# Performance work log

Measured on AMD Instinct MI355X. Metric: run time of the kernel, lower is better.

## Reference

```python
import jax, jax.numpy as jnp
import numpy as np

NHEADS = 64; EMB = 2048; STATE = 128; KCONV = 4; NGROUPS = 1
HEAD_DIM = 64; CHUNK = 128; EPS = 1e-6
INTER = NHEADS * HEAD_DIM                  # int(expand*emb_dim) = 4096
CONV_DIM = INTER + 2 * NGROUPS * STATE     # 4352
PROJ = INTER + CONV_DIM + NHEADS           # 8512
BATCH = 2; SEQ = 2048


def segsum(x):
    # x: (..., T) -> (..., T, T) stable segment sums; -inf strictly above diagonal
    T = x.shape[-1]
    xe = jnp.broadcast_to(x[..., None], x.shape + (T,))
    m_strict = jnp.tril(jnp.ones((T, T), bool), -1)
    s = jnp.cumsum(jnp.where(m_strict, xe, 0.0), axis=-2)
    m_incl = jnp.tril(jnp.ones((T, T), bool), 0)
    return jnp.where(m_incl, s, -jnp.inf)


def setup_inputs() -> dict:
    key = jax.random.key(0)
    ks = jax.random.split(key, 6)
    x = jax.random.normal(ks[0], (BATCH, SEQ, EMB), jnp.float32)
    in_proj_w = jax.random.normal(ks[1], (PROJ, EMB), jnp.float32) * 0.02
    conv_w = jax.random.normal(ks[2], (CONV_DIM, 1, KCONV), jnp.float32) * 0.2
    conv_b = jax.random.normal(ks[3], (CONV_DIM,), jnp.float32) * 0.1
    dt_bias = jnp.ones((NHEADS,), jnp.float32)
    A_log = jnp.log(jnp.arange(1, NHEADS + 1, dtype=jnp.float32))
    D = jnp.ones((NHEADS,), jnp.float32)
    norm_w = jnp.ones((INTER,), jnp.float32)
    out_proj_w = jax.random.normal(ks[4], (EMB, INTER), jnp.float32) * 0.02
    mask = jnp.ones((BATCH, 1, SEQ), jnp.int32)  # shape[1]==1 -> masking is a no-op, as in torch path
    return {"x": x, "in_proj_w": in_proj_w, "conv_w": conv_w, "conv_b": conv_b,
            "dt_bias": dt_bias, "A_log": A_log, "D": D, "norm_w": norm_w,
            "out_proj_w": out_proj_w, "mask": mask}


def reference(x, in_proj_w, conv_w, conv_b, dt_bias, A_log, D, norm_w, out_proj_w, mask):
    b, s, _ = x.shape
    proj = x @ in_proj_w.T                                    # (b,s,PROJ)
    gate = proj[..., :INTER]
    hBC = proj[..., INTER:INTER + CONV_DIM]
    dt = proj[..., INTER + CONV_DIM:]                         # (b,s,H)

    # causal depthwise conv1d (torch pads k-1 both sides then truncates to seq_len == left-pad k-1)
    conv = jax.lax.conv_general_dilated(
        hBC.transpose(0, 2, 1), conv_w, (1,), [(KCONV - 1, 0)],
        feature_group_count=CONV_DIM)
    hBC = jax.nn.silu((conv + conv_b[None, :, None]).transpose(0, 2, 1))

    hid = hBC[..., :INTER]
    Bm = hBC[..., INTER:INTER + NGROUPS * STATE]
    Cm = hBC[..., INTER + NGROUPS * STATE:]

    A = -jnp.exp(A_log)                                       # (H,)
    dt = jax.nn.softplus(dt + dt_bias)                        # clamp(0,inf) is a no-op after softplus

    hid = hid.reshape(b, s, NHEADS, HEAD_DIM)
    pad = (CHUNK - s % CHUNK) % CHUNK
    D_res = D[:, None] * jnp.pad(hid, ((0, 0), (0, pad), (0, 0), (0, 0)))
    hid = hid * dt[..., None]
    A_s = A * dt                                              # (b,s,H)
    Bm = jnp.tile(Bm.reshape(b, s, NGROUPS, STATE), (1, 1, NHEADS // NGROUPS, 1))
    Cm = jnp.tile(Cm.reshape(b, s, NGROUPS, STATE), (1, 1, NHEADS // NGROUPS, 1))

    def chunkify(t):
        t = jnp.pad(t, ((0, 0), (0, pad)) + ((0, 0),) * (t.ndim - 2))
        return t.reshape(b, -1, CHUNK, *t.shape[2:])

    hid_c, A_c, B_c, C_c = (chunkify(t) for t in (hid, A_s, Bm, Cm))
    A_c = A_c.transpose(0, 3, 1, 2)                           # (b,H,c,l)
    A_cum = jnp.cumsum(A_c, -1)

    # intra-chunk (diagonal blocks)
    L = jnp.exp(segsum(A_c))                                  # (b,H,c,l,l)
    G = jnp.einsum('bclhn,bcshn->bhcls', C_c, B_c)
    Y_diag = jnp.einsum('bhcls,bcshp->bclhp', G * L, hid_c)

    # per-chunk end states
    decay_states = jnp.exp(A_cum[..., -1:] - A_cum)           # (b,H,c,l)
    states = jnp.einsum('bclhn,bhcl,bclhp->bchpn', B_c, decay_states, hid_c)

    # inter-chunk recurrence
    A_last = jnp.pad(A_cum[..., -1], ((0, 0), (0, 0), (1, 0)))  # (b,H,c+1)
    decay_chunk = jnp.exp(segsum(A_last))                     # (b,H,c+1,c+1)
    states = jnp.concatenate([jnp.zeros_like(states[:, :1]), states], axis=1)
    new_states = jnp.einsum('bhzc,bchpn->bzhpn', decay_chunk, states)
    states = new_states[:, :-1]                               # states entering each chunk

    # off-diagonal (cross-chunk) contribution
    state_decay = jnp.exp(A_cum)                              # (b,H,c,l)
    Y_off = jnp.einsum('bclhn,bchpn,bhcl->bclhp', C_c, states, state_decay)

    y = (Y_diag + Y_off).reshape(b, -1, NHEADS, HEAD_DIM) + D_res
    y = y[:, :s].reshape(b, s, INTER)

    # gated RMSNorm
    yg = y * jax.nn.silu(gate)
    yn = norm_w * (yg * jax.lax.rsqrt(jnp.mean(yg * yg, -1, keepdims=True) + EPS))
    return yn @ out_proj_w.T
```

## Files before the change

kernel.cpp:

```cpp
#include <hip/hip_runtime.h>
#include <math.h>

#define NHEADS   64
#define EMB      2048
#define STATE    128
#define KCONV    4
#define HEAD_DIM 64
#define CHUNK    128
#define SEQL     2048
#define NBATCH   2
#define NCH      (SEQL/CHUNK)
#define INTER    (NHEADS*HEAD_DIM)
#define CONVD    (INTER + 2*STATE)
#define PROJD    (INTER + CONVD + NHEADS)
#define ROWS     (NBATCH*SEQL)
#define EPSV     1e-6f

__device__ __forceinline__ float sigmoidf_(float x){ return 1.f/(1.f+__expf(-x)); }

__device__ __forceinline__ float b2f(ushort u){
  union{float f; unsigned u;} x; x.u = ((unsigned)u)<<16; return x.f;
}
__device__ __forceinline__ ushort f2b(float f){
  union{float f; unsigned u;} x; x.f=f;
  unsigned r = x.u + 0x7FFFu + ((x.u>>16)&1u);
  return (ushort)(r>>16);
}
__device__ __forceinline__ float4 ld4(const float* p){ return *(const float4*)p; }
__device__ __forceinline__ float4 ld4(const ushort* p){
  ushort4 v = *(const ushort4*)p;
  return make_float4(b2f(v.x),b2f(v.y),b2f(v.z),b2f(v.w));
}
__device__ __forceinline__ void st4(float* p, float4 v){ *(float4*)p = v; }
__device__ __forceinline__ void st4(ushort* p, float4 v){
  ushort4 o; o.x=f2b(v.x); o.y=f2b(v.y); o.z=f2b(v.z); o.w=f2b(v.w);
  *(ushort4*)p = o;
}
__device__ __forceinline__ void stc(float* p, float v){ *p = v; }
__device__ __forceinline__ void stc(ushort* p, float v){ *p = f2b(v); }

__global__ __launch_bounds__(256) void f32_to_bf16_kernel(
    const float* __restrict__ in, ushort* __restrict__ out, long n)
{
  long i = ((long)blockIdx.x*256 + threadIdx.x) * 8;
  if (i >= n) return;
  float4 a = *(const float4*)(in + i);
  float4 b = *(const float4*)(in + i + 4);
  st4(out + i, a);
  st4(out + i + 4, b);
}

typedef __attribute__((ext_vector_type(8))) short short8v;
typedef __attribute__((ext_vector_type(4))) float float4v;

#define GLL16(g, l) __builtin_amdgcn_global_load_lds( \
    (const __attribute__((address_space(1))) void*)(g), \
    (__attribute__((address_space(3))) void*)(l), 16, 0, 0)

template<typename TC>
__global__ __launch_bounds__(256) void gemm_mfma_bt(
    const ushort* __restrict__ A, int lda,
    const ushort* __restrict__ B, int ldb,
    TC* __restrict__ C, int ldc,
    int N, int K)
{
  __shared__ ushort As[2][128*32];
  __shared__ ushort Bs[2][128*32];
  const int t = threadIdx.x;
  const int lt = t & 63, w = t >> 6;
  const int wr = w >> 1, wc = w & 1;

  const int nwg = gridDim.x * gridDim.y;
  int orig = blockIdx.x + gridDim.x * blockIdx.y;
  int tile = orig;
  if ((nwg & 7) == 0) tile = (orig & 7) * (nwg >> 3) + (orig >> 3);
  const int m0 = (tile / gridDim.x) * 128;
  const int n0 = (tile % gridDim.x) * 128;

  float4v acc[4][4];
  #pragma unroll
  for (int i=0;i<4;++i)
    #pragma unroll
    for (int j=0;j<4;++j) acc[i][j] = float4v{0.f,0.f,0.f,0.f};

  const int srow = t >> 2;
  const int scol = ((t & 3) ^ ((srow >> 1) & 3)) * 8;
  const int bn0 = min(n0 + srow, N-1);
  const int bn1 = min(n0 + 64 + srow, N-1);
  const long aoff0 = (long)(m0 + srow) * lda + scol;
  const long aoff1 = (long)(m0 + 64 + srow) * lda + scol;
  const long boff0 = (long)bn0 * ldb + scol;
  const long boff1 = (long)bn1 * ldb + scol;
  const int lr = lt & 15, lks = lt >> 4;

  for (int k0 = 0; k0 < K; k0 += 64) {
    GLL16(A + aoff0 + k0,      As[0] + t*8);
    GLL16(A + aoff1 + k0,      As[0] + 2048 + t*8);
    GLL16(B + boff0 + k0,      Bs[0] + t*8);
    GLL16(B + boff1 + k0,      Bs[0] + 2048 + t*8);
    GLL16(A + aoff0 + k0 + 32, As[1] + t*8);
    GLL16(A + aoff1 + k0 + 32, As[1] + 2048 + t*8);
    GLL16(B + boff0 + k0 + 32, Bs[1] + t*8);
    GLL16(B + boff1 + k0 + 32, Bs[1] + 2048 + t*8);
    __syncthreads();
    #pragma unroll
    for (int hB = 0; hB < 2; ++hB) {
      short8v af[4], bf[4];
      #pragma unroll
      for (int i = 0; i < 4; ++i) {
        int ra = wr*64 + i*16 + lr;
        af[i] = *(const short8v*)(As[hB] + ra*32 + ((lks ^ ((ra>>1)&3)) << 3));
        int rb = wc*64 + i*16 + lr;
        bf[i] = *(const short8v*)(Bs[hB] + rb*32 + ((lks ^ ((rb>>1)&3)) << 3));
      }
      #pragma unroll
      for (int i = 0; i < 4; ++i)
        #pragma unroll
        for (int j = 0; j < 4; ++j)
          acc[i][j] = __builtin_amdgcn_mfma_f32_16x16x32_bf16(af[i], bf[j], acc[i][j], 0, 0, 0);
    }
    __syncthreads();
  }

  const int cr = (lt >> 4) * 4;
  const int cc = lt & 15;
  #pragma unroll
  for (int i = 0; i < 4; ++i) {
    #pragma unroll
    for (int j = 0; j < 4; ++j) {
      int col = n0 + wc*64 + j*16 + cc;
      if (col < N) {
        #pragma unroll
        for (int r = 0; r < 4; ++r) {
          int row = m0 + wr*64 + i*16 + cr + r;
          stc(C + (long)row*ldc + col, acc[i][j][r]);
        }
      }
    }
  }
}

__global__ __launch_bounds__(256) void g_mfma_kernel(
    const ushort* __restrict__ conv, float* __restrict__ G)
{
  const int bc = blockIdx.x;
  const long r0 = (long)bc*CHUNK;
  __shared__ ushort Cs[128][136];
  __shared__ ushort Bs[128][136];
  const int t = threadIdx.x;
  const int lt = t & 63, w = t >> 6;
  const int lr = lt & 15, lk = (lt >> 4) * 8;

  for (int i = t; i < 128*16; i += 256) {
    int r = i >> 4, n0 = (i & 15) * 8;
    *(short8v*)&Cs[r][n0] = *(const short8v*)(conv + (r0+r)*CONVD + INTER + STATE + n0);
    *(short8v*)&Bs[r][n0] = *(const short8v*)(conv + (r0+r)*CONVD + INTER + n0);
  }
  __syncthreads();

  float4v acc[2][8];
  #pragma unroll
  for (int m=0;m<2;++m)
    #pragma unroll
    for (int j=0;j<8;++j) acc[m][j] = float4v{0,0,0,0};
  #pragma unroll
  for (int kk = 0; kk < 4; ++kk) {
    short8v a0 = *(const short8v*)&Cs[w*32 +      lr][kk*32 + lk];
    short8v a1 = *(const short8v*)&Cs[w*32 + 16 + lr][kk*32 + lk];
    #pragma unroll
    for (int nj = 0; nj < 8; ++nj) {
      short8v bv = *(const short8v*)&Bs[nj*16 + lr][kk*32 + lk];
      acc[0][nj] = __builtin_amdgcn_mfma_f32_16x16x32_bf16(a0, bv, acc[0][nj], 0, 0, 0);
      acc[1][nj] = __builtin_amdgcn_mfma_f32_16x16x32_bf16(a1, bv, acc[1][nj], 0, 0, 0);
    }
  }
  float* Gb = G + (long)bc*CHUNK*CHUNK;
  const int cr = (lt >> 4) * 4, cc = lt & 15;
  #pragma unroll
  for (int m = 0; m < 2; ++m)
    #pragma unroll
    for (int nj = 0; nj < 8; ++nj)
      #pragma unroll
      for (int r = 0; r < 4; ++r)
        Gb[(w*32 + m*16 + cr + r)*CHUNK + nj*16 + cc] = acc[m][nj][r];
}

__global__ __launch_bounds__(256) void conv_silu_kernel(
    const ushort* __restrict__ proj, const float* __restrict__ cw,
    const float* __restrict__ cb, ushort* __restrict__ out)
{
  const int C4 = CONVD/4;
  long idx = (long)blockIdx.x*256 + threadIdx.x;
  if (idx >= (long)ROWS*C4) return;
  int r = (int)(idx / C4);
  int c = (int)(idx % C4) * 4;
  int tt = r & (SEQL-1);
  float4 bv = *(const float4*)(cb + c);
  float acc0=bv.x, acc1=bv.y, acc2=bv.z, acc3=bv.w;
  float4 w0 = *(const float4*)(cw + (c+0)*KCONV);
  float4 w1 = *(const float4*)(cw + (c+1)*KCONV);
  float4 w2 = *(const float4*)(cw + (c+2)*KCONV);
  float4 w3 = *(const float4*)(cw + (c+3)*KCONV);
  const float wj0[4] = {w0.x,w0.y,w0.z,w0.w};
  const float wj1[4] = {w1.x,w1.y,w1.z,w1.w};
  const float wj2[4] = {w2.x,w2.y,w2.z,w2.w};
  const float wj3[4] = {w3.x,w3.y,w3.z,w3.w};
  #pragma unroll
  for (int j = 0; j < KCONV; ++j) {
    int tr = tt - (KCONV-1) + j;
    if (tr >= 0) {
      float4 v = ld4(proj + (long)(r - (KCONV-1) + j)*PROJD + INTER + c);
      acc0 = fmaf(v.x, wj0[j], acc0);
      acc1 = fmaf(v.y, wj1[j], acc1);
      acc2 = fmaf(v.z, wj2[j], acc2);
      acc3 = fmaf(v.w, wj3[j], acc3);
    }
  }
  float4 o;
  o.x = acc0 * sigmoidf_(acc0);
  o.y = acc1 * sigmoidf_(acc1);
  o.z = acc2 * sigmoidf_(acc2);
  o.w = acc3 * sigmoidf_(acc3);
  st4(out + (long)r*CONVD + c, o);
}

__global__ __launch_bounds__(256) void dt_acum_kernel(
    const ushort* __restrict__ proj, const float* __restrict__ dt_bias,
    const float* __restrict__ A_log, float* __restrict__ dtb,
    float* __restrict__ acum)
{
  const int bc = blockIdx.x;
  const long r0 = (long)bc*CHUNK;
  __shared__ float dts[CHUNK][NHEADS+1];
  const int t = threadIdx.x;
  for (int i = t; i < CHUNK*8; i += 256) {
    int l = i >> 3, h0 = (i & 7) * 8;
    short8v v = *(const short8v*)(proj + (r0+l)*PROJD + INTER + CONVD + h0);
    #pragma unroll
    for (int j = 0; j < 8; ++j) {
      float xv = b2f((ushort)v[j]) + dt_bias[h0+j];
      float sp = fmaxf(xv, 0.f) + __logf(1.f + __expf(-fabsf(xv)));
      dts[l][h0+j] = sp;
      dtb[(r0+l)*NHEADS + h0 + j] = sp;
    }
  }
  __syncthreads();
  if (t < NHEADS) {
    float Ah = -__expf(A_log[t]);
    float acc = 0.f;
    float* o = acum + ((long)bc*NHEADS + t)*CHUNK;
    for (int l = 0; l < CHUNK; ++l) { acc = fmaf(Ah, dts[l][t], acc); o[l] = acc; }
  }
}

__global__ __launch_bounds__(256) void states_mfma_kernel(
    const ushort* __restrict__ conv, const float* __restrict__ dtb,
    const float* __restrict__ acum, ushort* __restrict__ states)
{
  const int h = blockIdx.x, c = blockIdx.y, b = blockIdx.z;
  const int bc = b*NCH + c;
  const long r0 = (long)bc*CHUNK;
  __shared__ ushort Ahi[64][136];
  __shared__ ushort Alo[64][136];
  __shared__ ushort Bt[128][136];
  __shared__ float arow[CHUNK];
  __shared__ float wrow[CHUNK];
  const int t = threadIdx.x;
  const int lt = t & 63, w = t >> 6;
  const int lr = lt & 15, lk = (lt >> 4) * 8;

  if (t < CHUNK) arow[t] = acum[((long)bc*NHEADS + h)*CHUNK + t];
  __syncthreads();
  if (t < CHUNK) wrow[t] = dtb[(r0 + t)*NHEADS + h] * __expf(arow[CHUNK-1] - arow[t]);
  __syncthreads();

  for (int i = t; i < CHUNK*HEAD_DIM/8; i += 256) {
    int l = i >> 3, p0 = (i & 7) * 8;
    short8v v = *(const short8v*)(conv + (r0+l)*CONVD + h*HEAD_DIM + p0);
    float wl = wrow[l];
    #pragma unroll
    for (int j = 0; j < 8; ++j) {
      float f = b2f((ushort)v[j]) * wl;
      ushort hb = f2b(f);
      Ahi[p0+j][l] = hb;
      Alo[p0+j][l] = f2b(f - b2f(hb));
    }
  }
  for (int i = t; i < CHUNK*STATE/8; i += 256) {
    int l = i >> 4, n0 = (i & 15) * 8;
    short8v v = *(const short8v*)(conv + (r0+l)*CONVD + INTER + n0);
    #pragma unroll
    for (int j = 0; j < 8; ++j) Bt[n0+j][l] = (ushort)v[j];
  }
  __syncthreads();

  float4v acc[8];
  #pragma unroll
  for (int j = 0; j < 8; ++j) acc[j] = float4v{0,0,0,0};
  #pragma unroll
  for (int kk = 0; kk < 4; ++kk) {
    short8v ahi = *(const short8v*)&Ahi[w*16 + lr][kk*32 + lk];
    short8v alo = *(const short8v*)&Alo[w*16 + lr][kk*32 + lk];
    #pragma unroll
    for (int nj = 0; nj < 8; ++nj) {
      short8v bv = *(const short8v*)&Bt[nj*16 + lr][kk*32 + lk];
      acc[nj] = __builtin_amdgcn_mfma_f32_16x16x32_bf16(ahi, bv, acc[nj], 0, 0, 0);
      acc[nj] = __builtin_amdgcn_mfma_f32_16x16x32_bf16(alo, bv, acc[nj], 0, 0, 0);
    }
  }
  ushort* so = states + ((long)bc*NHEADS + h)*HEAD_DIM*STATE;
  const int cr = (lt >> 4) * 4, cc = lt & 15;
  #pragma unroll
  for (int nj = 0; nj < 8; ++nj)
    #pragma unroll
    for (int r = 0; r < 4; ++r)
      so[(w*16 + cr + r)*STATE + nj*16 + cc] = f2b(acc[nj][r]);
}

__global__ __launch_bounds__(256) void scan_kernel(
    ushort* __restrict__ states, const float* __restrict__ acum)
{
  const int blk = blockIdx.x;
  const int bh = blk >> 2, pq = blk & 3;
  const int b = bh >> 6, h = bh & 63;
  const int t = threadIdx.x;
  const int base = pq * 16 * STATE;
  float acc[8];
  #pragma unroll
  for (int i=0;i<8;++i) acc[i]=0.f;
  for (int c = 0; c < NCH; ++c) {
    const long bch = ((long)(b*NCH + c)*NHEADS + h);
    float lam = __expf(acum[bch*CHUNK + CHUNK-1]);
    ushort* sb = states + bch*HEAD_DIM*STATE + base;
    #pragma unroll
    for (int i = 0; i < 8; ++i) {
      float v = b2f(sb[t + i*256]);
      sb[t + i*256] = f2b(acc[i]);
      acc[i] = fmaf(acc[i], lam, v);
    }
  }
}

__global__ __launch_bounds__(256) void y_mfma_kernel(
    const ushort* __restrict__ conv, const float* __restrict__ dtb,
    const float* __restrict__ acum, const float* __restrict__ G,
    const ushort* __restrict__ states, const float* __restrict__ Dp,
    ushort* __restrict__ proj)
{
  const int h = blockIdx.x;
  const int c = blockIdx.y >> 1, mh = blockIdx.y & 1;
  const int b = blockIdx.z;
  const int bc = b*NCH + c;
  const int mbase = mh * 64;
  const long r0 = (long)bc*CHUNK;

  __shared__ float  Af[64][132];
  __shared__ ushort B0[64][136];
  __shared__ ushort B1[64][136];
  __shared__ float arow[CHUNK];
  __shared__ float dtr[CHUNK];
  __shared__ float el[64];

  const int t = threadIdx.x;
  const int lt = t & 63, w = t >> 6;
  const int lr = lt & 15, lk = (lt >> 4) * 8;

  if (t < CHUNK) {
    arow[t] = acum[((long)bc*NHEADS + h)*CHUNK + t];
    dtr[t]  = dtb[(r0 + t)*NHEADS + h];
  }
  __syncthreads();

  if (t < 64) el[t] = __expf(arow[mbase + t]);
  for (int i = t; i < CHUNK*HEAD_DIM/8; i += 256) {
    int s = i >> 3, p0 = (i & 7) * 8;
    short8v v = *(const short8v*)(conv + (r0+s)*CONVD + h*HEAD_DIM + p0);
    #pragma unroll
    for (int j = 0; j < 8; ++j) B0[p0+j][s] = (ushort)v[j];
  }
  {
    const ushort* stb = states + ((long)bc*NHEADS + h)*HEAD_DIM*STATE;
    for (int i = t; i < HEAD_DIM*STATE/8; i += 256) {
      int p = i >> 4, n0 = (i & 15) * 8;
      *(short8v*)&B1[p][n0] = *(const short8v*)(stb + p*STATE + n0);
    }
  }
  {
    const float* Gb = G + (long)bc*CHUNK*CHUNK;
    for (int i = t; i < 64*CHUNK; i += 256) {
      int ll = i >> 7, s = i & 127;
      int l = mbase + ll;
      float wv = 0.f;
      if (s <= l) wv = Gb[l*CHUNK + s] * __expf(arow[l] - arow[s]) * dtr[s];
      Af[ll][s] = wv;
    }
  }
  __syncthreads();

  float4v acc1[4], acc2[4];
  #pragma unroll
  for (int j = 0; j < 4; ++j) { acc1[j] = float4v{0,0,0,0}; acc2[j] = float4v{0,0,0,0}; }

  #pragma unroll
  for (int kk = 0; kk < 4; ++kk) {
    const float* ap = &Af[w*16 + lr][kk*32 + lk];
    float a8[8];
    *(float4*)&a8[0] = *(const float4*)ap;
    *(float4*)&a8[4] = *(const float4*)(ap + 4);
    short8v ahi, alo;
    #pragma unroll
    for (int e = 0; e < 8; ++e) {
      ushort hb = f2b(a8[e]);
      float rem = a8[e] - b2f(hb);
      ahi[e] = (short)hb;
      alo[e] = (short)f2b(rem);
    }
    #pragma unroll
    for (int nj = 0; nj < 4; ++nj) {
      short8v bfv = *(const short8v*)&B0[nj*16 + lr][kk*32 + lk];
      acc1[nj] = __builtin_amdgcn_mfma_f32_16x16x32_bf16(ahi, bfv, acc1[nj], 0, 0, 0);
      acc1[nj] = __builtin_amdgcn_mfma_f32_16x16x32_bf16(alo, bfv, acc1[nj], 0, 0, 0);
    }
  }
  __syncthreads();

  for (int i = t; i < 64*STATE; i += 256) {
    int ll = i >> 7, n = i & 127;
    Af[ll][n] = b2f(conv[(r0 + mbase + ll)*CONVD + INTER + STATE + n]);
  }
  __syncthreads();

  #pragma unroll
  for (int kk = 0; kk < 4; ++kk) {
    const float* ap = &Af[w*16 + lr][kk*32 + lk];
    float a8[8];
    *(float4*)&a8[0] = *(const float4*)ap;
    *(float4*)&a8[4] = *(const float4*)(ap + 4);
    short8v ahi;
    #pragma unroll
    for (int e = 0; e < 8; ++e) ahi[e] = (short)f2b(a8[e]);
    #pragma unroll
    for (int nj = 0; nj < 4; ++nj) {
      short8v bfv = *(const short8v*)&B1[nj*16 + lr][kk*32 + lk];
      acc2[nj] = __builtin_amdgcn_mfma_f32_16x16x32_bf16(ahi, bfv, acc2[nj], 0, 0, 0);
    }
  }

  const float Dh = Dp[h];
  const int cr = (lt >> 4) * 4, cc = lt & 15;
  #pragma unroll
  for (int nj = 0; nj < 4; ++nj) {
    int p = nj*16 + cc;
    #pragma unroll
    for (int r = 0; r < 4; ++r) {
      int ll = w*16 + cr + r;
      float hid_raw = b2f(B0[p][mbase + ll]);
      float yv = acc1[nj][r] + el[ll]*acc2[nj][r] + Dh*hid_raw;
      proj[(r0 + mbase + ll)*PROJD + INTER + h*HEAD_DIM + p] = f2b(yv);
    }
  }
}

__global__ __launch_bounds__(256) void gate_norm_kernel(
    ushort* __restrict__ proj, const float* __restrict__ nw)
{
  const int r = blockIdx.x;
  const int t = threadIdx.x;
  __shared__ float red[256];
  ushort* gate = proj + (long)r*PROJD;
  ushort* y = gate + INTER;
  float vals[16];
  float ss = 0.f;
  #pragma unroll
  for (int k = 0; k < 4; ++k) {
    int j = (t + k*256) * 4;
    float4 g = ld4(gate + j);
    float4 yv = ld4(y + j);
    float v0 = yv.x * g.x * sigmoidf_(g.x);
    float v1 = yv.y * g.y * sigmoidf_(g.y);
    float v2 = yv.z * g.z * sigmoidf_(g.z);
    float v3 = yv.w * g.w * sigmoidf_(g.w);
    vals[k*4+0]=v0; vals[k*4+1]=v1; vals[k*4+2]=v2; vals[k*4+3]=v3;
    ss += v0*v0 + v1*v1 + v2*v2 + v3*v3;
  }
  red[t] = ss;
  __syncthreads();
  for (int sft = 128; sft > 0; sft >>= 1) {
    if (t < sft) red[t] += red[t+sft];
    __syncthreads();
  }
  float scale = rsqrtf(red[0] / (float)INTER + EPSV);
  #pragma unroll
  for (int k = 0; k < 4; ++k) {
    int j = (t + k*256) * 4;
    float4 w = *(const float4*)(nw + j);
    st4(y + j, make_float4(vals[k*4+0]*scale*w.x, vals[k*4+1]*scale*w.y,
                           vals[k*4+2]*scale*w.z, vals[k*4+3]*scale*w.w));
  }
}

extern "C" void kernel_launch(void* const* d_in, const int* in_sizes, int n_in,
                              void* d_out, int out_size, void* d_ws, size_t ws_size,
                              hipStream_t stream) {
  const float* x       = (const float*)d_in[0];
  const float* Wi      = (const float*)d_in[1];
  const float* cw      = (const float*)d_in[2];
  const float* cb      = (const float*)d_in[3];
  const float* dt_bias = (const float*)d_in[4];
  const float* A_log   = (const float*)d_in[5];
  const float* Dp      = (const float*)d_in[6];
  const float* nw      = (const float*)d_in[7];
  const float* Wo      = (const float*)d_in[8];
  float* out = (float*)d_out;

  ushort* projb = (ushort*)d_ws;
  ushort* R     = projb + (size_t)ROWS*PROJD;
  ushort* xb    = R;
  ushort* Wib   = R + (size_t)ROWS*EMB;
  ushort* Wob   = R;
  ushort* convb = R;
  float*  dtb   = (float*)(convb + (size_t)ROWS*CONVD);
  float*  acum  = dtb  + (size_t)ROWS*NHEADS;
  float*  Gb    = acum + (size_t)NBATCH*NCH*NHEADS*CHUNK;
  ushort* st    = (ushort*)(Gb + (size_t)NBATCH*NCH*CHUNK*CHUNK);

  size_t need = (size_t)ROWS*PROJD*2 + (size_t)ROWS*CONVD*2
              + (size_t)ROWS*NHEADS*4 + (size_t)NBATCH*NCH*NHEADS*CHUNK*4
              + (size_t)NBATCH*NCH*CHUNK*CHUNK*4
              + (size_t)NBATCH*NCH*NHEADS*HEAD_DIM*STATE*2;
  if (ws_size < need) return;

  f32_to_bf16_kernel<<<(int)((long)ROWS*EMB/8/256), 256, 0, stream>>>(x, xb, (long)ROWS*EMB);
  f32_to_bf16_kernel<<<(int)((long)PROJD*EMB/8/256), 256, 0, stream>>>(Wi, Wib, (long)PROJD*EMB);
  gemm_mfma_bt<ushort><<<dim3((PROJD+127)/128, ROWS/128), 256, 0, stream>>>(
      xb, EMB, Wib, EMB, projb, PROJD, PROJD, EMB);
  conv_silu_kernel<<<(int)(((long)ROWS*(CONVD/4)+255)/256), 256, 0, stream>>>(
      projb, cw, cb, convb);
  dt_acum_kernel<<<NBATCH*NCH, 256, 0, stream>>>(projb, dt_bias, A_log, dtb, acum);
  g_mfma_kernel<<<NBATCH*NCH, 256, 0, stream>>>(convb, Gb);
  states_mfma_kernel<<<dim3(NHEADS, NCH, NBATCH), 256, 0, stream>>>(convb, dtb, acum, st);
  scan_kernel<<<NBATCH*NHEADS*4, 256, 0, stream>>>(st, acum);
  y_mfma_kernel<<<dim3(NHEADS, NCH*2, NBATCH), 256, 0, stream>>>(
      convb, dtb, acum, Gb, st, Dp, projb);
  gate_norm_kernel<<<ROWS, 256, 0, stream>>>(projb, nw);
  f32_to_bf16_kernel<<<(int)((long)EMB*INTER/8/256), 256, 0, stream>>>(Wo, Wob, (long)EMB*INTER);
  gemm_mfma_bt<float><<<dim3(EMB/128, ROWS/128), 256, 0, stream>>>(
      projb + INTER, PROJD, Wob, INTER, out, EMB, EMB, INTER);
}
```

Baseline: 590.2 us.

## Vectorize MFMA epilogue stores, merge conversions, fold y kernel halves

Swaps the MFMA operand order in every matmul so each lane holds four consecutive output columns, which lets the epilogues issue one vector store instead of four scalar ones. The two fp32-to-bf16 conversions for x and the input weights are merged into a single launch. The y kernel now processes a whole chunk per block, loading the per-head operands once for both 64-row halves, and skips the causally zero K-steps in the first half. The cost is fewer blocks and more serialized work per block in the y kernel.

```diff
diff --git a/kernel.cpp b/kernel.cpp
--- a/kernel.cpp
+++ b/kernel.cpp
@@ -36,22 +36,43 @@
   ushort4 o; o.x=f2b(v.x); o.y=f2b(v.y); o.z=f2b(v.z); o.w=f2b(v.w);
   *(ushort4*)p = o;
 }
-__device__ __forceinline__ void stc(float* p, float v){ *p = v; }
-__device__ __forceinline__ void stc(ushort* p, float v){ *p = f2b(v); }
+
+typedef __attribute__((ext_vector_type(8))) short short8v;
+typedef __attribute__((ext_vector_type(4))) float float4v;
+
+__device__ __forceinline__ void stv4(float* p, float4v v){
+  *(float4*)p = make_float4(v[0],v[1],v[2],v[3]);
+}
+__device__ __forceinline__ void stv4(ushort* p, float4v v){
+  ushort4 o; o.x=f2b(v[0]); o.y=f2b(v[1]); o.z=f2b(v[2]); o.w=f2b(v[3]);
+  *(ushort4*)p = o;
+}
+
+__global__ __launch_bounds__(256) void conv2_bf16_kernel(
+    const float* __restrict__ a, ushort* __restrict__ oa, long na,
+    const float* __restrict__ b, ushort* __restrict__ ob, long nb)
+{
+  long i = ((long)blockIdx.x*256 + threadIdx.x) * 8;
+  if (i < na) {
+    st4(oa + i, *(const float4*)(a + i));
+    st4(oa + i + 4, *(const float4*)(a + i + 4));
+  } else {
+    long j = i - na;
+    if (j < nb) {
+      st4(ob + j, *(const float4*)(b + j));
+      st4(ob + j + 4, *(const float4*)(b + j + 4));
+    }
+  }
+}
 
 __global__ __launch_bounds__(256) void f32_to_bf16_kernel(
     const float* __restrict__ in, ushort* __restrict__ out, long n)
 {
   long i = ((long)blockIdx.x*256 + threadIdx.x) * 8;
   if (i >= n) return;
-  float4 a = *(const float4*)(in + i);
-  float4 b = *(const float4*)(in + i + 4);
-  st4(out + i, a);
-  st4(out + i + 4, b);
-}
-
-typedef __attribute__((ext_vector_type(8))) short short8v;
-typedef __attribute__((ext_vector_type(4))) float float4v;
+  st4(out + i, *(const float4*)(in + i));
+  st4(out + i + 4, *(const float4*)(in + i + 4));
+}
 
 #define GLL16(g, l) __builtin_amdgcn_global_load_lds( \
     (const __attribute__((address_space(1))) void*)(g), \
@@ -117,25 +138,20 @@
       for (int i = 0; i < 4; ++i)
         #pragma unroll
         for (int j = 0; j < 4; ++j)
-          acc[i][j] = __builtin_amdgcn_mfma_f32_16x16x32_bf16(af[i], bf[j], acc[i][j], 0, 0, 0);
+          acc[i][j] = __builtin_amdgcn_mfma_f32_16x16x32_bf16(bf[j], af[i], acc[i][j], 0, 0, 0);
     }
     __syncthreads();
   }
 
-  const int cr = (lt >> 4) * 4;
-  const int cc = lt & 15;
+  const int cm = lt & 15;
+  const int cn4 = (lt >> 4) * 4;
   #pragma unroll
   for (int i = 0; i < 4; ++i) {
+    int row = m0 + wr*64 + i*16 + cm;
     #pragma unroll
     for (int j = 0; j < 4; ++j) {
-      int col = n0 + wc*64 + j*16 + cc;
-      if (col < N) {
-        #pragma unroll
-        for (int r = 0; r < 4; ++r) {
-          int row = m0 + wr*64 + i*16 + cr + r;
-          stc(C + (long)row*ldc + col, acc[i][j][r]);
-        }
-      }
+      int col = n0 + wc*64 + j*16 + cn4;
+      if (col < N) stv4(C + (long)row*ldc + col, acc[i][j]);
     }
   }
 }
@@ -170,19 +186,19 @@
     #pragma unroll
     for (int nj = 0; nj < 8; ++nj) {
       short8v bv = *(const short8v*)&Bs[nj*16 + lr][kk*32 + lk];
-      acc[0][nj] = __builtin_amdgcn_mfma_f32_16x16x32_bf16(a0, bv, acc[0][nj], 0, 0, 0);
-      acc[1][nj] = __builtin_amdgcn_mfma_f32_16x16x32_bf16(a1, bv, acc[1][nj], 0, 0, 0);
+      acc[0][nj] = __builtin_amdgcn_mfma_f32_16x16x32_bf16(bv, a0, acc[0][nj], 0, 0, 0);
+      acc[1][nj] = __builtin_amdgcn_mfma_f32_16x16x32_bf16(bv, a1, acc[1][nj], 0, 0, 0);
     }
   }
   float* Gb = G + (long)bc*CHUNK*CHUNK;
-  const int cr = (lt >> 4) * 4, cc = lt & 15;
-  #pragma unroll
-  for (int m = 0; m < 2; ++m)
+  const int cl = lt & 15, cs4 = (lt >> 4) * 4;
+  #pragma unroll
+  for (int m = 0; m < 2; ++m) {
+    int l = w*32 + m*16 + cl;
     #pragma unroll
     for (int nj = 0; nj < 8; ++nj)
-      #pragma unroll
-      for (int r = 0; r < 4; ++r)
-        Gb[(w*32 + m*16 + cr + r)*CHUNK + nj*16 + cc] = acc[m][nj][r];
+      stv4(Gb + l*CHUNK + nj*16 + cs4, acc[m][nj]);
+  }
 }
 
 __global__ __launch_bounds__(256) void conv_silu_kernel(
@@ -304,17 +320,16 @@
     #pragma unroll
     for (int nj = 0; nj < 8; ++nj) {
       short8v bv = *(const short8v*)&Bt[nj*16 + lr][kk*32 + lk];
-      acc[nj] = __builtin_amdgcn_mfma_f32_16x16x32_bf16(ahi, bv, acc[nj], 0, 0, 0);
-      acc[nj] = __builtin_amdgcn_mfma_f32_16x16x32_bf16(alo, bv, acc[nj], 0, 0, 0);
+      acc[nj] = __builtin_amdgcn_mfma_f32_16x16x32_bf16(bv, ahi, acc[nj], 0, 0, 0);
+      acc[nj] = __builtin_amdgcn_mfma_f32_16x16x32_bf16(bv, alo, acc[nj], 0, 0, 0);
     }
   }
   ushort* so = states + ((long)bc*NHEADS + h)*HEAD_DIM*STATE;
-  const int cr = (lt >> 4) * 4, cc = lt & 15;
+  const int cp = lt & 15, cn4 = (lt >> 4) * 4;
+  const int p = w*16 + cp;
   #pragma unroll
   for (int nj = 0; nj < 8; ++nj)
-    #pragma unroll
-    for (int r = 0; r < 4; ++r)
-      so[(w*16 + cr + r)*STATE + nj*16 + cc] = f2b(acc[nj][r]);
+    stv4(so + p*STATE + nj*16 + cn4, acc[nj]);
 }
 
 __global__ __launch_bounds__(256) void scan_kernel(
@@ -347,11 +362,8 @@
     const ushort* __restrict__ states, const float* __restrict__ Dp,
     ushort* __restrict__ proj)
 {
-  const int h = blockIdx.x;
-  const int c = blockIdx.y >> 1, mh = blockIdx.y & 1;
-  const int b = blockIdx.z;
+  const int h = blockIdx.x, c = blockIdx.y, b = blockIdx.z;
   const int bc = b*NCH + c;
-  const int mbase = mh * 64;
   const long r0 = (long)bc*CHUNK;
 
   __shared__ float  Af[64][132];
@@ -359,7 +371,7 @@
   __shared__ ushort B1[64][136];
   __shared__ float arow[CHUNK];
   __shared__ float dtr[CHUNK];
-  __shared__ float el[64];
+  __shared__ float el[CHUNK];
 
   const int t = threadIdx.x;
   const int lt = t & 63, w = t >> 6;
@@ -371,7 +383,7 @@
   }
   __syncthreads();
 
-  if (t < 64) el[t] = __expf(arow[mbase + t]);
+  if (t < CHUNK) el[t] = __expf(arow[t]);
   for (int i = t; i < CHUNK*HEAD_DIM/8; i += 256) {
     int s = i >> 3, p0 = (i & 7) * 8;
     short8v v = *(const short8v*)(conv + (r0+s)*CONVD + h*HEAD_DIM + p0);
@@ -387,76 +399,95 @@
   }
   {
     const float* Gb = G + (long)bc*CHUNK*CHUNK;
-    for (int i = t; i < 64*CHUNK; i += 256) {
-      int ll = i >> 7, s = i & 127;
-      int l = mbase + ll;
+    for (int i = t; i < 64*64; i += 256) {
+      int ll = i >> 6, s = i & 63;
       float wv = 0.f;
-      if (s <= l) wv = Gb[l*CHUNK + s] * __expf(arow[l] - arow[s]) * dtr[s];
+      if (s <= ll) wv = Gb[ll*CHUNK + s] * __expf(arow[ll] - arow[s]) * dtr[s];
       Af[ll][s] = wv;
     }
   }
   __syncthreads();
 
-  float4v acc1[4], acc2[4];
-  #pragma unroll
-  for (int j = 0; j < 4; ++j) { acc1[j] = float4v{0,0,0,0}; acc2[j] = float4v{0,0,0,0}; }
-
-  #pragma unroll
-  for (int kk = 0; kk < 4; ++kk) {
-    const float* ap = &Af[w*16 + lr][kk*32 + lk];
-    float a8[8];
-    *(float4*)&a8[0] = *(const float4*)ap;
-    *(float4*)&a8[4] = *(const float4*)(ap + 4);
-    short8v ahi, alo;
-    #pragma unroll
-    for (int e = 0; e < 8; ++e) {
-      ushort hb = f2b(a8[e]);
-      float rem = a8[e] - b2f(hb);
-      ahi[e] = (short)hb;
-      alo[e] = (short)f2b(rem);
-    }
+  const float Dh = Dp[h];
+  const int cl = lt & 15, cp4 = (lt >> 4) * 4;
+
+  #pragma unroll
+  for (int mh = 0; mh < 2; ++mh) {
+    const int mbase = mh * 64;
+    if (mh == 1) {
+      __syncthreads();
+      const float* Gb = G + (long)bc*CHUNK*CHUNK;
+      for (int i = t; i < 64*CHUNK; i += 256) {
+        int ll = i >> 7, s = i & 127;
+        int l = 64 + ll;
+        float wv = 0.f;
+        if (s <= l) wv = Gb[l*CHUNK + s] * __expf(arow[l] - arow[s]) * dtr[s];
+        Af[ll][s] = wv;
+      }
+      __syncthreads();
+    }
+
+    float4v acc1[4], acc2[4];
+    #pragma unroll
+    for (int j = 0; j < 4; ++j) { acc1[j] = float4v{0,0,0,0}; acc2[j] = float4v{0,0,0,0}; }
+
+    const int kkmax = mh ? 4 : 2;
+    for (int kk = 0; kk < kkmax; ++kk) {
+      const float* ap = &Af[w*16 + lr][kk*32 + lk];
+      float a8[8];
+      *(float4*)&a8[0] = *(const float4*)ap;
+      *(float4*)&a8[4] = *(const float4*)(ap + 4);
+      short8v ahi, alo;
+      #pragma unroll
+      for (int e = 0; e < 8; ++e) {
+        ushort hb = f2b(a8[e]);
+        float rem = a8[e] - b2f(hb);
+        ahi[e] = (short)hb;
+        alo[e] = (short)f2b(rem);
+      }
+      #pragma unroll
+      for (int nj = 0; nj < 4; ++nj) {
+        short8v bfv = *(const short8v*)&B0[nj*16 + lr][kk*32 + lk];
+        acc1[nj] = __builtin_amdgcn_mfma_f32_16x16x32_bf16(bfv, ahi, acc1[nj], 0, 0, 0);
+        acc1[nj] = __builtin_amdgcn_mfma_f32_16x16x32_bf16(bfv, alo, acc1[nj], 0, 0, 0);
+      }
+    }
+    __syncthreads();
+
+    for (int i = t; i < 64*STATE; i += 256) {
+      int ll = i >> 7, n = i & 127;
+      Af[ll][n] = b2f(conv[(r0 + mbase + ll)*CONVD + INTER + STATE + n]);
+    }
+    __syncthreads();
+
+    #pragma unroll
+    for (int kk = 0; kk < 4; ++kk) {
+      const float* ap = &Af[w*16 + lr][kk*32 + lk];
+      float a8[8];
+      *(float4*)&a8[0] = *(const float4*)ap;
+      *(float4*)&a8[4] = *(const float4*)(ap + 4);
+      short8v ahi;
+      #pragma unroll
+      for (int e = 0; e < 8; ++e) ahi[e] = (short)f2b(a8[e]);
+      #pragma unroll
+      for (int nj = 0; nj < 4; ++nj) {
+        short8v bfv = *(const short8v*)&B1[nj*16 + lr][kk*32 + lk];
+        acc2[nj] = __builtin_amdgcn_mfma_f32_16x16x32_bf16(bfv, ahi, acc2[nj], 0, 0, 0);
+      }
+    }
+
+    const int ll = w*16 + cl;
+    const float elv = el[mbase + ll];
     #pragma unroll
     for (int nj = 0; nj < 4; ++nj) {
-      short8v bfv = *(const short8v*)&B0[nj*16 + lr][kk*32 + lk];
-      acc1[nj] = __builtin_amdgcn_mfma_f32_16x16x32_bf16(ahi, bfv, acc1[nj], 0, 0, 0);
-      acc1[nj] = __builtin_amdgcn_mfma_f32_16x16x32_bf16(alo, bfv, acc1[nj], 0, 0, 0);
-    }
-  }
-  __syncthreads();
-
-  for (int i = t; i < 64*STATE; i += 256) {
-    int ll = i >> 7, n = i & 127;
-    Af[ll][n] = b2f(conv[(r0 + mbase + ll)*CONVD + INTER + STATE + n]);
-  }
-  __syncthreads();
-
-  #pragma unroll
-  for (int kk = 0; kk < 4; ++kk) {
-    const float* ap = &Af[w*16 + lr][kk*32 + lk];
-    float a8[8];
-    *(float4*)&a8[0] = *(const float4*)ap;
-    *(float4*)&a8[4] = *(const float4*)(ap + 4);
-    short8v ahi;
-    #pragma unroll
-    for (int e = 0; e < 8; ++e) ahi[e] = (short)f2b(a8[e]);
-    #pragma unroll
-    for (int nj = 0; nj < 4; ++nj) {
-      short8v bfv = *(const short8v*)&B1[nj*16 + lr][kk*32 + lk];
-      acc2[nj] = __builtin_amdgcn_mfma_f32_16x16x32_bf16(ahi, bfv, acc2[nj], 0, 0, 0);
-    }
-  }
-
-  const float Dh = Dp[h];
-  const int cr = (lt >> 4) * 4, cc = lt & 15;
-  #pragma unroll
-  for (int nj = 0; nj < 4; ++nj) {
-    int p = nj*16 + cc;
-    #pragma unroll
-    for (int r = 0; r < 4; ++r) {
-      int ll = w*16 + cr + r;
-      float hid_raw = b2f(B0[p][mbase + ll]);
-      float yv = acc1[nj][r] + el[ll]*acc2[nj][r] + Dh*hid_raw;
-      proj[(r0 + mbase + ll)*PROJD + INTER + h*HEAD_DIM + p] = f2b(yv);
+      int p0 = nj*16 + cp4;
+      float4v yv;
+      #pragma unroll
+      for (int r = 0; r < 4; ++r) {
+        float hid_raw = b2f(B0[p0 + r][mbase + ll]);
+        yv[r] = acc1[nj][r] + elv*acc2[nj][r] + Dh*hid_raw;
+      }
+      stv4(proj + (r0 + mbase + ll)*PROJD + INTER + h*HEAD_DIM + p0, yv);
     }
   }
 }
@@ -530,8 +561,10 @@
               + (size_t)NBATCH*NCH*NHEADS*HEAD_DIM*STATE*2;
   if (ws_size < need) return;
 
-  f32_to_bf16_kernel<<<(int)((long)ROWS*EMB/8/256), 256, 0, stream>>>(x, xb, (long)ROWS*EMB);
-  f32_to_bf16_kernel<<<(int)((long)PROJD*EMB/8/256), 256, 0, stream>>>(Wi, Wib, (long)PROJD*EMB);
+  {
+    long na = (long)ROWS*EMB, nb = (long)PROJD*EMB;
+    conv2_bf16_kernel<<<(int)((na+nb)/8/256), 256, 0, stream>>>(x, xb, na, Wi, Wib, nb);
+  }
   gemm_mfma_bt<ushort><<<dim3((PROJD+127)/128, ROWS/128), 256, 0, stream>>>(
       xb, EMB, Wib, EMB, projb, PROJD, PROJD, EMB);
   conv_silu_kernel<<<(int)(((long)ROWS*(CONVD/4)+255)/256), 256, 0, stream>>>(
@@ -540,7 +573,7 @@
   g_mfma_kernel<<<NBATCH*NCH, 256, 0, stream>>>(convb, Gb);
   states_mfma_kernel<<<dim3(NHEADS, NCH, NBATCH), 256, 0, stream>>>(convb, dtb, acum, st);
   scan_kernel<<<NBATCH*NHEADS*4, 256, 0, stream>>>(st, acum);
-  y_mfma_kernel<<<dim3(NHEADS, NCH*2, NBATCH), 256, 0, stream>>>(
+  y_mfma_kernel<<<dim3(NHEADS, NCH, NBATCH), 256, 0, stream>>>(
       convb, dtb, acum, Gb, st, Dp, projb);
   gate_norm_kernel<<<ROWS, 256, 0, stream>>>(projb, nw);
   f32_to_bf16_kernel<<<(int)((long)EMB*INTER/8/256), 256, 0, stream>>>(Wo, Wob, (long)EMB*INTER);
```

Result: no change. 579.1 us (-1.9%).
